# Kernel tuning notes

Measured on AMD Instinct MI355X. Metric: run time of the kernel, lower is better.

## Reference

```python
import jax, jax.numpy as jnp
import numpy as np

B, T, D, N = 16, 1024, 1024, 64
H = D // N          # 16 heads
DW, DA, DG = 64, 64, 160   # fla RWKV7 LoRA dims for D=1024
EPS = 64e-5         # GroupNorm eps = head_dim * 1e-5


def setup_inputs() -> dict:
    key = jax.random.key(0)
    ks = iter(jax.random.split(key, 40))
    def nrm(shape, s=0.02):
        return jax.random.normal(next(ks), shape, dtype=jnp.float32) * s
    inp = {
        "x": jax.random.normal(next(ks), (B, T, D), dtype=jnp.float32),
        # token-shift mixing coefficients
        "x_r": nrm((D,)), "x_w": nrm((D,)), "x_k": nrm((D,)),
        "x_v": nrm((D,)), "x_a": nrm((D,)), "x_g": nrm((D,)),
        # projections (no bias)
        "W_r": nrm((D, D)), "W_k": nrm((D, D)), "W_v": nrm((D, D)), "W_o": nrm((D, D)),
        # decay LoRA
        "w0": nrm((D,)), "w1": nrm((D, DW)), "w2": nrm((DW, D)),
        # in-context-lr LoRA
        "a0": nrm((D,)), "a1": nrm((D, DA)), "a2": nrm((DA, D)),
        # gate LoRA
        "g1": nrm((D, DG)), "g2": nrm((DG, D)),
        # per-channel key modifiers and per-head bonus
        "k_k": jnp.ones((D,), jnp.float32) * 0.85,
        "k_a": jnp.ones((D,), jnp.float32),
        "r_k": nrm((H, N)),
        # per-head GroupNorm affine
        "gn_w": jnp.ones((D,), jnp.float32), "gn_b": jnp.zeros((D,), jnp.float32),
        # classifier head
        "W_cls": nrm((D, 2)), "b_cls": jnp.zeros((2,), jnp.float32),
    }
    return inp


def rwkv7_scan(r, w, k, v, a, b):
    """RWKV7 delta-rule recurrence. All inputs [B,T,H,N]. Returns [B,T,H,N].
    S_t = S_{t-1} * diag(exp(-exp(w_t))) + (S_{t-1} a_t) b_t^T + v_t k_t^T
    o_t = S_t r_t
    """
    decay = jnp.exp(-jnp.exp(w))
    def step(S, inp):
        r_t, d_t, k_t, v_t, a_t, b_t = inp  # each [B,H,N]
        sa = jnp.einsum('bhij,bhj->bhi', S, a_t)
        S = (S * d_t[:, :, None, :]
             + sa[..., None] * b_t[:, :, None, :]
             + v_t[..., None] * k_t[:, :, None, :])
        o_t = jnp.einsum('bhij,bhj->bhi', S, r_t)
        return S, o_t
    xs = tuple(jnp.moveaxis(u, 1, 0) for u in (r, decay, k, v, a, b))
    S0 = jnp.zeros((r.shape[0], H, N, N), jnp.float32)
    _, o = jax.lax.scan(step, S0, xs)
    return jnp.moveaxis(o, 0, 1)


def reference(x, x_r, x_w, x_k, x_v, x_a, x_g,
              W_r, W_k, W_v, W_o,
              w0, w1, w2, a0, a1, a2, g1, g2,
              k_k, k_a, r_k, gn_w, gn_b, W_cls, b_cls):
    Bx, Tx, Dx = x.shape
    # token shift: delta = x_{t-1} - x_t (x_{-1} = 0)
    xprev = jnp.pad(x, ((0, 0), (1, 0), (0, 0)))[:, :-1]
    delta = xprev - x
    xr = x + delta * x_r
    xw = x + delta * x_w
    xk = x + delta * x_k
    xv = x + delta * x_v
    xa = x + delta * x_a
    xg = x + delta * x_g

    r = xr @ W_r
    k = xk @ W_k
    v = xv @ W_v   # layer 0: v_first = v, no value-residual mixing
    w = -jax.nn.softplus(-(w0 + jnp.tanh(xw @ w1) @ w2)) - 0.5
    a = jax.nn.sigmoid(a0 + (xa @ a1) @ a2)
    g = jax.nn.sigmoid(xg @ g1) @ g2

    kk = (k * k_k).reshape(Bx, Tx, H, N)
    kk = kk / jnp.maximum(jnp.linalg.norm(kk, axis=-1, keepdims=True), 1e-12)
    k = k * (1.0 + (a - 1.0) * k_a)

    rh = r.reshape(Bx, Tx, H, N)
    kh = k.reshape(Bx, Tx, H, N)
    vh = v.reshape(Bx, Tx, H, N)
    ah = a.reshape(Bx, Tx, H, N)
    wh = w.reshape(Bx, Tx, H, N)

    o = rwkv7_scan(rh, wh, kh, vh, -kk, kk * ah)

    # per-head GroupNorm (num_groups = H over channels D)
    mu = o.mean(-1, keepdims=True)
    var = o.var(-1, keepdims=True)
    o = (o - mu) / jnp.sqrt(var + EPS)
    o = o * gn_w.reshape(H, N) + gn_b.reshape(H, N)

    # per-head bonus term
    o = o + (rh * kh * r_k).sum(-1, keepdims=True) * vh
    o = (o.reshape(Bx, Tx, Dx) * g) @ W_o

    # TextRWKV head: max-pool over time, relu, (dropout=eval noop), linear
    h = jax.nn.relu(jnp.max(o, axis=1))
    return h @ W_cls + b_cls
```

## Files before the change

kernel.cpp:

```cpp
#include <hip/hip_runtime.h>
#include <hip/hip_bf16.h>

typedef unsigned short u16;
typedef unsigned int u32;

#define Bb 16
#define Tt 1024
#define Dd 1024
#define Nn 64
#define Hh 16
#define Mm (Bb*Tt)

#define TILE_M 64
#define TILE_N 64
#define TILE_K 16

typedef float f32x4 __attribute__((ext_vector_type(4)));
typedef short s16x8 __attribute__((ext_vector_type(8)));

struct __align__(8) u16x4s { u16 x, y, z, w; };

__device__ __forceinline__ float bf2f(u16 u) { return __uint_as_float(((u32)u) << 16); }
__device__ __forceinline__ u16 f2bf(float f) {
    __hip_bfloat16 h = __float2bfloat16(f);
    return *reinterpret_cast<u16*>(&h);
}
__device__ __forceinline__ float sigf(float x) { return 1.0f / (1.0f + expf(-x)); }

__global__ __launch_bounds__(256)
void mix6_kernel(const float* __restrict__ x,
                 const float* __restrict__ cr, const float* __restrict__ ck,
                 const float* __restrict__ cv, const float* __restrict__ cw,
                 const float* __restrict__ ca, const float* __restrict__ cg,
                 u16* __restrict__ o0, u16* __restrict__ o1, u16* __restrict__ o2,
                 u16* __restrict__ o3, u16* __restrict__ o4, u16* __restrict__ o5)
{
    const int m = blockIdx.x;
    const int c0 = threadIdx.x * 4;
    const size_t base = (size_t)m * Dd + c0;
    float4 xc = *(const float4*)(x + base);
    float4 xp = make_float4(0.f, 0.f, 0.f, 0.f);
    if (m & (Tt - 1)) xp = *(const float4*)(x + base - Dd);
    float dx[4] = {xp.x - xc.x, xp.y - xc.y, xp.z - xc.z, xp.w - xc.w};
    float xv[4] = {xc.x, xc.y, xc.z, xc.w};
    const float* cfs[6] = {cr, ck, cv, cw, ca, cg};
    u16* outs[6] = {o0, o1, o2, o3, o4, o5};
#pragma unroll
    for (int s = 0; s < 6; ++s) {
        float4 cf = *(const float4*)(cfs[s] + c0);
        float c4[4] = {cf.x, cf.y, cf.z, cf.w};
        u16x4s ov;
        u16* op = &ov.x;
#pragma unroll
        for (int l = 0; l < 4; ++l) op[l] = f2bf(fmaf(dx[l], c4[l], xv[l]));
        *(u16x4s*)(outs[s] + base) = ov;
    }
}

__global__ __launch_bounds__(256)
void sgemm_small(const u16* __restrict__ A, int lda,
                 const float* __restrict__ Bw, int ldb,
                 u16* __restrict__ C, int ldc,
                 int N, int K, int act)
{
    __shared__ float As[TILE_K][TILE_M + 1];
    __shared__ float Bs[TILE_K][TILE_N + 1];
    const int tid = threadIdx.x;
    const int tx = tid & 15, ty = tid >> 4;
    const int bm = blockIdx.x * TILE_M;
    const int bn = blockIdx.y * TILE_N;

    float acc[4][4] = {};

    for (int k0 = 0; k0 < K; k0 += TILE_K) {
#pragma unroll
        for (int l = 0; l < 4; ++l) {
            int idx = l * 256 + tid;
            int kk = idx & 15, mm = idx >> 4;
            As[kk][mm] = bf2f(A[(size_t)(bm + mm) * lda + k0 + kk]);
        }
#pragma unroll
        for (int l = 0; l < 4; ++l) {
            int idx = l * 256 + tid;
            int nn = idx & 63, kk = idx >> 6;
            int gn = bn + nn;
            Bs[kk][nn] = (gn < N) ? Bw[(size_t)(k0 + kk) * ldb + gn] : 0.0f;
        }
        __syncthreads();
#pragma unroll
        for (int kk = 0; kk < TILE_K; ++kk) {
            float af[4], bf[4];
#pragma unroll
            for (int i = 0; i < 4; ++i) af[i] = As[kk][ty * 4 + i];
#pragma unroll
            for (int j = 0; j < 4; ++j) bf[j] = Bs[kk][tx * 4 + j];
#pragma unroll
            for (int i = 0; i < 4; ++i)
#pragma unroll
                for (int j = 0; j < 4; ++j)
                    acc[i][j] = fmaf(af[i], bf[j], acc[i][j]);
        }
        __syncthreads();
    }

#pragma unroll
    for (int i = 0; i < 4; ++i) {
        int gm = bm + ty * 4 + i;
#pragma unroll
        for (int j = 0; j < 4; ++j) {
            int gn = bn + tx * 4 + j;
            if (gn >= N) continue;
            float v = acc[i][j];
            if (act == 1) v = tanhf(v);
            else if (act == 2) v = sigf(v);
            C[(size_t)gm * ldc + gn] = f2bf(v);
        }
    }
}

template<int ACT, bool HAS_BIAS>
__global__ __launch_bounds__(256)
void gemm_mfma(const u16* __restrict__ A, int lda,
               const float* __restrict__ W,
               const float* __restrict__ bias,
               u16* __restrict__ C, int K)
{
    __shared__ u16 As[128][40];
    __shared__ u16 Bs[128][40];
    const int tid = threadIdx.x;
    const int bm = blockIdx.x * 128, bn = blockIdx.y * 128;
    const int lane = tid & 63, w = tid >> 6;
    const int wr = w >> 1, wc = w & 1;
    const int lr = lane & 15, kg = lane >> 4;

    f32x4 acc[4][4];
#pragma unroll
    for (int m = 0; m < 4; ++m)
#pragma unroll
        for (int n = 0; n < 4; ++n) acc[m][n] = (f32x4){0.f, 0.f, 0.f, 0.f};

    for (int k0 = 0; k0 < K; k0 += 32) {
        {
            int row = tid >> 2, part = tid & 3;
            *(s16x8*)&As[row][part * 8] =
                *(const s16x8*)(A + (size_t)(bm + row) * lda + k0 + part * 8);
            row += 64;
            *(s16x8*)&As[row][part * 8] =
                *(const s16x8*)(A + (size_t)(bm + row) * lda + k0 + part * 8);
        }
        {
            int n4 = (tid & 31) * 4;
            int kp = tid >> 5;
#pragma unroll
            for (int it = 0; it < 2; ++it) {
                int k = 2 * (kp + it * 8);
                const float* wp = W + (size_t)(k0 + k) * 1024 + bn + n4;
                float4 wa = *(const float4*)wp;
                float4 wb = *(const float4*)(wp + 1024);
                *(u32*)&Bs[n4 + 0][k] = (u32)f2bf(wa.x) | ((u32)f2bf(wb.x) << 16);
                *(u32*)&Bs[n4 + 1][k] = (u32)f2bf(wa.y) | ((u32)f2bf(wb.y) << 16);
                *(u32*)&Bs[n4 + 2][k] = (u32)f2bf(wa.z) | ((u32)f2bf(wb.z) << 16);
                *(u32*)&Bs[n4 + 3][k] = (u32)f2bf(wa.w) | ((u32)f2bf(wb.w) << 16);
            }
        }
        __syncthreads();
        s16x8 af[4], bfr[4];
#pragma unroll
        for (int m = 0; m < 4; ++m)
            af[m] = *(const s16x8*)&As[wr * 64 + m * 16 + lr][kg * 8];
#pragma unroll
        for (int n = 0; n < 4; ++n)
            bfr[n] = *(const s16x8*)&Bs[wc * 64 + n * 16 + lr][kg * 8];
#pragma unroll
        for (int m = 0; m < 4; ++m)
#pragma unroll
            for (int n = 0; n < 4; ++n)
                acc[m][n] = __builtin_amdgcn_mfma_f32_16x16x32_bf16(af[m], bfr[n], acc[m][n], 0, 0, 0);
        __syncthreads();
    }

#pragma unroll
    for (int n = 0; n < 4; ++n) {
        int col = bn + wc * 64 + n * 16 + lr;
        float bv = HAS_BIAS ? bias[col] : 0.0f;
#pragma unroll
        for (int m = 0; m < 4; ++m) {
            int row0 = bm + wr * 64 + m * 16 + kg * 4;
#pragma unroll
            for (int r = 0; r < 4; ++r) {
                float v = acc[m][n][r] + bv;
                if (ACT == 2) v = sigf(v);
                else if (ACT == 3) {
                    float ww = -log1pf(expf(-v)) - 0.5f;
                    v = expf(-expf(ww));
                }
                C[(size_t)(row0 + r) * 1024 + col] = f2bf(v);
            }
        }
    }
}

__global__ __launch_bounds__(256)
void gemm_wo_mfma(const u16* __restrict__ A,
                  const float* __restrict__ W,
                  float* __restrict__ Hbuf)
{
    __shared__ u16 As[128][40];
    __shared__ u16 Bs[128][40];
    const int tid = threadIdx.x;
    const int bm = blockIdx.x * 128, bn = blockIdx.y * 128;
    const int lane = tid & 63, w = tid >> 6;
    const int wr = w >> 1, wc = w & 1;
    const int lr = lane & 15, kg = lane >> 4;

    f32x4 acc[4][4];
#pragma unroll
    for (int m = 0; m < 4; ++m)
#pragma unroll
        for (int n = 0; n < 4; ++n) acc[m][n] = (f32x4){0.f, 0.f, 0.f, 0.f};

    for (int k0 = 0; k0 < 1024; k0 += 32) {
        {
            int row = tid >> 2, part = tid & 3;
            *(s16x8*)&As[row][part * 8] =
                *(const s16x8*)(A + (size_t)(bm + row) * 1024 + k0 + part * 8);
            row += 64;
            *(s16x8*)&As[row][part * 8] =
                *(const s16x8*)(A + (size_t)(bm + row) * 1024 + k0 + part * 8);
        }
        {
            int n4 = (tid & 31) * 4;
            int kp = tid >> 5;
#pragma unroll
            for (int it = 0; it < 2; ++it) {
                int k = 2 * (kp + it * 8);
                const float* wp = W + (size_t)(k0 + k) * 1024 + bn + n4;
                float4 wa = *(const float4*)wp;
                float4 wb = *(const float4*)(wp + 1024);
                *(u32*)&Bs[n4 + 0][k] = (u32)f2bf(wa.x) | ((u32)f2bf(wb.x) << 16);
                *(u32*)&Bs[n4 + 1][k] = (u32)f2bf(wa.y) | ((u32)f2bf(wb.y) << 16);
                *(u32*)&Bs[n4 + 2][k] = (u32)f2bf(wa.z) | ((u32)f2bf(wb.z) << 16);
                *(u32*)&Bs[n4 + 3][k] = (u32)f2bf(wa.w) | ((u32)f2bf(wb.w) << 16);
            }
        }
        __syncthreads();
        s16x8 af[4], bfr[4];
#pragma unroll
        for (int m = 0; m < 4; ++m)
            af[m] = *(const s16x8*)&As[wr * 64 + m * 16 + lr][kg * 8];
#pragma unroll
        for (int n = 0; n < 4; ++n)
            bfr[n] = *(const s16x8*)&Bs[wc * 64 + n * 16 + lr][kg * 8];
#pragma unroll
        for (int m = 0; m < 4; ++m)
#pragma unroll
            for (int n = 0; n < 4; ++n)
                acc[m][n] = __builtin_amdgcn_mfma_f32_16x16x32_bf16(af[m], bfr[n], acc[m][n], 0, 0, 0);
        __syncthreads();
    }

    const int b = bm >> 10;
#pragma unroll
    for (int n = 0; n < 4; ++n) {
        float mv = -1e30f;
#pragma unroll
        for (int m = 0; m < 4; ++m)
#pragma unroll
            for (int r = 0; r < 4; ++r) mv = fmaxf(mv, acc[m][n][r]);
        mv = fmaxf(mv, __shfl_xor(mv, 16));
        mv = fmaxf(mv, __shfl_xor(mv, 32));
        mv = fmaxf(mv, 0.0f);
        if (lane < 16) {
            int col = bn + wc * 64 + n * 16 + lr;
            atomicMax((u32*)&Hbuf[b * Dd + col], __float_as_uint(mv));
        }
    }
}

__global__ __launch_bounds__(256)
void ew_kv_kernel(u16* __restrict__ kbuf, u16* __restrict__ abuf,
                  u16* __restrict__ kkbuf,
                  const float* __restrict__ k_k, const float* __restrict__ k_a)
{
    const int m = blockIdx.x;
    const int tid = threadIdx.x;
    const int c0 = tid * 4;
    const size_t base = (size_t)m * Dd + c0;
    u16x4s kv4 = *(const u16x4s*)(kbuf + base);
    u16x4s av4 = *(const u16x4s*)(abuf + base);
    float4 kkc = *(const float4*)(k_k + c0);
    float4 kac = *(const float4*)(k_a + c0);

    float kin[4] = {bf2f(kv4.x), bf2f(kv4.y), bf2f(kv4.z), bf2f(kv4.w)};
    float ain[4] = {bf2f(av4.x), bf2f(av4.y), bf2f(av4.z), bf2f(av4.w)};
    float kkc4[4] = {kkc.x, kkc.y, kkc.z, kkc.w};
    float kac4[4] = {kac.x, kac.y, kac.z, kac.w};

    float kr[4];
#pragma unroll
    for (int l = 0; l < 4; ++l) kr[l] = kin[l] * kkc4[l];
    float ss = kr[0]*kr[0] + kr[1]*kr[1] + kr[2]*kr[2] + kr[3]*kr[3];
#pragma unroll
    for (int mask = 1; mask < 16; mask <<= 1) ss += __shfl_xor(ss, mask);
    float inv = 1.0f / fmaxf(sqrtf(ss), 1e-12f);

    u16x4s kkv, kmv, bvv;
    u16* kkp = &kkv.x; u16* kmp = &kmv.x; u16* bvp = &bvv.x;
#pragma unroll
    for (int l = 0; l < 4; ++l) {
        float kkf = kr[l] * inv;
        kkp[l] = f2bf(kkf);
        kmp[l] = f2bf(kin[l] * (1.0f + (ain[l] - 1.0f) * kac4[l]));
        bvp[l] = f2bf(kkf * ain[l]);
    }
    *(u16x4s*)(kkbuf + base) = kkv;
    *(u16x4s*)(kbuf  + base) = kmv;
    *(u16x4s*)(abuf  + base) = bvv;
}

__global__ __launch_bounds__(256)
void scan_kernel(const u16* __restrict__ rb, const u16* __restrict__ db,
                 const u16* __restrict__ kb, const u16* __restrict__ vb,
                 const u16* __restrict__ kkb, const u16* __restrict__ bvb,
                 u16* __restrict__ ob)
{
    const int blk = blockIdx.x;
    const int batch = blk >> 4, head = blk & 15;
    const int tid = threadIdx.x;
    const int w = tid >> 6;
    const int lane = tid & 63;
    const int q = lane & 3, il = lane >> 2;
    const int i = w * 16 + il;
    const int j0 = q * 16;

    __shared__ float ws[4][2][6][64];

    const size_t rowbase = (size_t)batch * Tt * Dd + head * Nn;

    float S[16];
#pragma unroll
    for (int jj = 0; jj < 16; ++jj) S[jj] = 0.0f;

    {
        size_t off = rowbase + lane;
        ws[w][0][0][lane] = bf2f(rb[off]);
        ws[w][0][1][lane] = bf2f(db[off]);
        ws[w][0][2][lane] = bf2f(kb[off]);
        ws[w][0][3][lane] = bf2f(vb[off]);
        ws[w][0][4][lane] = bf2f(kkb[off]);
        ws[w][0][5][lane] = bf2f(bvb[off]);
    }
    u16 p0 = 0, p1 = 0, p2 = 0, p3 = 0, p4 = 0, p5 = 0;
    {
        size_t off = rowbase + Dd + lane;
        p0 = rb[off]; p1 = db[off]; p2 = kb[off];
        p3 = vb[off]; p4 = kkb[off]; p5 = bvb[off];
    }

    int c = 0;
    for (int t = 0; t < Tt; ++t) {
        if (t + 1 < Tt) {
            ws[w][c ^ 1][0][lane] = bf2f(p0);
            ws[w][c ^ 1][1][lane] = bf2f(p1);
            ws[w][c ^ 1][2][lane] = bf2f(p2);
            ws[w][c ^ 1][3][lane] = bf2f(p3);
            ws[w][c ^ 1][4][lane] = bf2f(p4);
            ws[w][c ^ 1][5][lane] = bf2f(p5);
        }
        if (t + 2 < Tt) {
            size_t off = rowbase + (size_t)(t + 2) * Dd + lane;
            p0 = rb[off]; p1 = db[off]; p2 = kb[off];
            p3 = vb[off]; p4 = kkb[off]; p5 = bvb[off];
        }

        float rv[16], dec[16], kv[16], kkv[16], bv[16];
#pragma unroll
        for (int u = 0; u < 4; ++u) {
            *(float4*)&rv[u*4]  = *(const float4*)&ws[w][c][0][j0 + u*4];
            *(float4*)&dec[u*4] = *(const float4*)&ws[w][c][1][j0 + u*4];
            *(float4*)&kv[u*4]  = *(const float4*)&ws[w][c][2][j0 + u*4];
            *(float4*)&kkv[u*4] = *(const float4*)&ws[w][c][4][j0 + u*4];
            *(float4*)&bv[u*4]  = *(const float4*)&ws[w][c][5][j0 + u*4];
        }
        float vi = ws[w][c][3][i];

        float sa = 0.0f;
#pragma unroll
        for (int jj = 0; jj < 16; ++jj) sa = fmaf(S[jj], kkv[jj], sa);
        sa = -sa;
        sa += __shfl_xor(sa, 1);
        sa += __shfl_xor(sa, 2);

        float op = 0.0f;
#pragma unroll
        for (int jj = 0; jj < 16; ++jj) {
            float Sv = S[jj] * dec[jj];
            Sv = fmaf(sa, bv[jj], Sv);
            Sv = fmaf(vi, kv[jj], Sv);
            S[jj] = Sv;
            op = fmaf(Sv, rv[jj], op);
        }
        op += __shfl_xor(op, 1);
        op += __shfl_xor(op, 2);
        if (q == 0) ob[rowbase + (size_t)t * Dd + i] = f2bf(op);

        c ^= 1;
    }
}

__global__ __launch_bounds__(256)
void gn_kernel(const u16* __restrict__ ob, const u16* __restrict__ rb,
               const u16* __restrict__ kb, const u16* __restrict__ vb,
               const u16* __restrict__ gb,
               const float* __restrict__ gn_w, const float* __restrict__ gn_b,
               const float* __restrict__ r_k, u16* __restrict__ o2)
{
    const int m = blockIdx.x;
    const int tid = threadIdx.x;
    const int c0 = tid * 4;
    const int h = tid >> 4;
    const int jh = c0 & 63;
    const size_t base = (size_t)m * Dd + c0;

    u16x4s ov4 = *(const u16x4s*)(ob + base);
    u16x4s rv4 = *(const u16x4s*)(rb + base);
    u16x4s kv4 = *(const u16x4s*)(kb + base);
    u16x4s vv4 = *(const u16x4s*)(vb + base);
    u16x4s gv4 = *(const u16x4s*)(gb + base);
    float4 rkc = *(const float4*)(r_k + h * 64 + jh);

    float ovv[4] = {bf2f(ov4.x), bf2f(ov4.y), bf2f(ov4.z), bf2f(ov4.w)};
    float rv[4] = {bf2f(rv4.x), bf2f(rv4.y), bf2f(rv4.z), bf2f(rv4.w)};
    float kv[4] = {bf2f(kv4.x), bf2f(kv4.y), bf2f(kv4.z), bf2f(kv4.w)};
    float vv[4] = {bf2f(vv4.x), bf2f(vv4.y), bf2f(vv4.z), bf2f(vv4.w)};
    float gv[4] = {bf2f(gv4.x), bf2f(gv4.y), bf2f(gv4.z), bf2f(gv4.w)};
    float rk4[4] = {rkc.x, rkc.y, rkc.z, rkc.w};

    float s1 = ovv[0] + ovv[1] + ovv[2] + ovv[3];
    float s2 = ovv[0]*ovv[0] + ovv[1]*ovv[1] + ovv[2]*ovv[2] + ovv[3]*ovv[3];
    float sb = rv[0]*kv[0]*rk4[0] + rv[1]*kv[1]*rk4[1] + rv[2]*kv[2]*rk4[2] + rv[3]*kv[3]*rk4[3];
#pragma unroll
    for (int mask = 1; mask < 16; mask <<= 1) {
        s1 += __shfl_xor(s1, mask);
        s2 += __shfl_xor(s2, mask);
        sb += __shfl_xor(sb, mask);
    }
    float mu = s1 * (1.0f / 64.0f);
    float var = s2 * (1.0f / 64.0f) - mu * mu;
    float rstd = rsqrtf(var + 6.4e-4f);

    float4 gwv = *(const float4*)(gn_w + c0);
    float4 gbv = *(const float4*)(gn_b + c0);
    float gw4[4] = {gwv.x, gwv.y, gwv.z, gwv.w};
    float gb4[4] = {gbv.x, gbv.y, gbv.z, gbv.w};

    u16x4s outv; u16* op = &outv.x;
#pragma unroll
    for (int l = 0; l < 4; ++l) {
        float v = (((ovv[l] - mu) * rstd) * gw4[l] + gb4[l] + sb * vv[l]) * gv[l];
        op[l] = f2bf(v);
    }
    *(u16x4s*)(o2 + base) = outv;
}

__global__ __launch_bounds__(256)
void zero_kernel(float* __restrict__ p, int n)
{
    int i = blockIdx.x * 256 + threadIdx.x;
    if (i < n) p[i] = 0.0f;
}

__global__ __launch_bounds__(256)
void cls_kernel(const float* __restrict__ hp, const float* __restrict__ Wc,
                const float* __restrict__ bc, float* __restrict__ out)
{
    const int p = blockIdx.x;
    const int b = p >> 1, c = p & 1;
    const int tid = threadIdx.x;
    float partial = 0.0f;
    for (int d = tid; d < Dd; d += 256)
        partial = fmaf(hp[b * Dd + d], Wc[d * 2 + c], partial);
    __shared__ float red[256];
    red[tid] = partial;
    __syncthreads();
    for (int s = 128; s > 0; s >>= 1) {
        if (tid < s) red[tid] += red[tid + s];
        __syncthreads();
    }
    if (tid == 0) out[b * 2 + c] = red[0] + bc[c];
}

extern "C" void kernel_launch(void* const* d_in, const int* in_sizes, int n_in,
                              void* d_out, int out_size, void* d_ws, size_t ws_size,
                              hipStream_t stream)
{
    const float* x    = (const float*)d_in[0];
    const float* x_r  = (const float*)d_in[1];
    const float* x_w  = (const float*)d_in[2];
    const float* x_k  = (const float*)d_in[3];
    const float* x_v  = (const float*)d_in[4];
    const float* x_a  = (const float*)d_in[5];
    const float* x_g  = (const float*)d_in[6];
    const float* W_r  = (const float*)d_in[7];
    const float* W_k  = (const float*)d_in[8];
    const float* W_v  = (const float*)d_in[9];
    const float* W_o  = (const float*)d_in[10];
    const float* w0   = (const float*)d_in[11];
    const float* w1   = (const float*)d_in[12];
    const float* w2   = (const float*)d_in[13];
    const float* a0   = (const float*)d_in[14];
    const float* a1   = (const float*)d_in[15];
    const float* a2   = (const float*)d_in[16];
    const float* g1   = (const float*)d_in[17];
    const float* g2   = (const float*)d_in[18];
    const float* k_k  = (const float*)d_in[19];
    const float* k_a  = (const float*)d_in[20];
    const float* r_k  = (const float*)d_in[21];
    const float* gn_w = (const float*)d_in[22];
    const float* gn_b = (const float*)d_in[23];
    const float* Wcls = (const float*)d_in[24];
    const float* bcls = (const float*)d_in[25];
    float* out = (float*)d_out;

    const size_t MD = (size_t)Mm * Dd;
    char* w = (char*)d_ws;
    u16* S0 = (u16*)w; w += MD * 2;
    u16* S1 = (u16*)w; w += MD * 2;
    u16* S2 = (u16*)w; w += MD * 2;
    u16* S3 = (u16*)w; w += MD * 2;
    u16* S4 = (u16*)w; w += MD * 2;
    u16* S5 = (u16*)w; w += MD * 2;
    u16* S6 = (u16*)w; w += MD * 2;
    u16* TW = (u16*)w; w += (size_t)Mm * 64 * 2;
    u16* TA = (u16*)w; w += (size_t)Mm * 64 * 2;
    u16* TG = (u16*)w; w += (size_t)Mm * 160 * 2;
    float* bufH = (float*)w; w += (size_t)Bb * Dd * 4;

    dim3 blk(256);
    dim3 gMix(Mm);
    dim3 gMf(Mm / 128, 1024 / 128);
    dim3 g64(Mm / TILE_M, 1);
    dim3 g160(Mm / TILE_M, 3);

    mix6_kernel<<<gMix, blk, 0, stream>>>(x, x_r, x_k, x_v, x_w, x_a, x_g,
                                          S0, S1, S2, S3, S4, S5);
    sgemm_small<<<g64,  blk, 0, stream>>>(S3, Dd, w1, 64,  TW, 64,  64,  Dd, 1);
    sgemm_small<<<g64,  blk, 0, stream>>>(S4, Dd, a1, 64,  TA, 64,  64,  Dd, 0);
    sgemm_small<<<g160, blk, 0, stream>>>(S5, Dd, g1, 160, TG, 160, 160, Dd, 2);
    gemm_mfma<0, false><<<gMf, blk, 0, stream>>>(S0, Dd, W_r, nullptr, S3, Dd);
    gemm_mfma<0, false><<<gMf, blk, 0, stream>>>(S1, Dd, W_k, nullptr, S4, Dd);
    gemm_mfma<0, false><<<gMf, blk, 0, stream>>>(S2, Dd, W_v, nullptr, S5, Dd);
    gemm_mfma<3, true><<<gMf, blk, 0, stream>>>(TW, 64, w2, w0, S0, 64);
    gemm_mfma<2, true><<<gMf, blk, 0, stream>>>(TA, 64, a2, a0, S1, 64);
    ew_kv_kernel<<<Mm, blk, 0, stream>>>(S4, S1, S2, k_k, k_a);
    scan_kernel<<<Bb * Hh, blk, 0, stream>>>(S3, S0, S4, S5, S2, S1, S6);
    gemm_mfma<0, false><<<gMf, blk, 0, stream>>>(TG, 160, g2, nullptr, S0, 160);
    gn_kernel<<<Mm, blk, 0, stream>>>(S6, S3, S4, S5, S0, gn_w, gn_b, r_k, S2);
    zero_kernel<<<(Bb * Dd + 255) / 256, blk, 0, stream>>>(bufH, Bb * Dd);
    gemm_wo_mfma<<<gMf, blk, 0, stream>>>(S2, W_o, bufH);
    cls_kernel<<<32, blk, 0, stream>>>(bufH, Wcls, bcls, out);
}
```

Before: 1.941 ms.

## Load scan inputs directly into registers, dropping LDS staging

The RWKV7 scan kernel no longer stages each timestep's r/decay/k/v/kk/b vectors through shared memory. Each lane now loads its 16-element bf16 slices straight from global memory as 16-byte vector loads, prefetched two steps ahead in registers, and converts them inline. This removes the LDS write/read traffic and the per-step staging work from the serial recurrence loop. In exchange, each lane issues redundant global loads of the same data and needs more registers for the two-deep prefetch buffers.

```diff
diff --git a/kernel.cpp b/kernel.cpp
--- a/kernel.cpp
+++ b/kernel.cpp
@@ -19,6 +19,7 @@
 typedef short s16x8 __attribute__((ext_vector_type(8)));
 
 struct __align__(8) u16x4s { u16 x, y, z, w; };
+struct slice16 { s16x8 lo, hi; };
 
 __device__ __forceinline__ float bf2f(u16 u) { return __uint_as_float(((u32)u) << 16); }
 __device__ __forceinline__ u16 f2bf(float f) {
@@ -26,6 +27,13 @@
     return *reinterpret_cast<u16*>(&h);
 }
 __device__ __forceinline__ float sigf(float x) { return 1.0f / (1.0f + expf(-x)); }
+
+__device__ __forceinline__ slice16 ldslice(const u16* p) {
+    slice16 s;
+    s.lo = *(const s16x8*)p;
+    s.hi = *(const s16x8*)(p + 8);
+    return s;
+}
 
 __global__ __launch_bounds__(256)
 void mix6_kernel(const float* __restrict__ x,
@@ -333,78 +341,74 @@
     const int i = w * 16 + il;
     const int j0 = q * 16;
 
-    __shared__ float ws[4][2][6][64];
-
     const size_t rowbase = (size_t)batch * Tt * Dd + head * Nn;
 
     float S[16];
 #pragma unroll
     for (int jj = 0; jj < 16; ++jj) S[jj] = 0.0f;
 
+    slice16 cr, cd, ck_, cc, cb;
+    u16 cv;
     {
-        size_t off = rowbase + lane;
-        ws[w][0][0][lane] = bf2f(rb[off]);
-        ws[w][0][1][lane] = bf2f(db[off]);
-        ws[w][0][2][lane] = bf2f(kb[off]);
-        ws[w][0][3][lane] = bf2f(vb[off]);
-        ws[w][0][4][lane] = bf2f(kkb[off]);
-        ws[w][0][5][lane] = bf2f(bvb[off]);
-    }
-    u16 p0 = 0, p1 = 0, p2 = 0, p3 = 0, p4 = 0, p5 = 0;
-    {
-        size_t off = rowbase + Dd + lane;
-        p0 = rb[off]; p1 = db[off]; p2 = kb[off];
-        p3 = vb[off]; p4 = kkb[off]; p5 = bvb[off];
-    }
-
-    int c = 0;
+        size_t o = rowbase + j0;
+        cr = ldslice(rb + o); cd = ldslice(db + o); ck_ = ldslice(kb + o);
+        cc = ldslice(kkb + o); cb = ldslice(bvb + o);
+        cv = vb[rowbase + i];
+    }
+    slice16 nr = cr, nd = cd, nk = ck_, nc = cc, nb = cb;
+    u16 nv = cv;
+    if (Tt > 1) {
+        size_t o = rowbase + Dd + j0;
+        nr = ldslice(rb + o); nd = ldslice(db + o); nk = ldslice(kb + o);
+        nc = ldslice(kkb + o); nb = ldslice(bvb + o);
+        nv = vb[rowbase + Dd + i];
+    }
+
     for (int t = 0; t < Tt; ++t) {
-        if (t + 1 < Tt) {
-            ws[w][c ^ 1][0][lane] = bf2f(p0);
-            ws[w][c ^ 1][1][lane] = bf2f(p1);
-            ws[w][c ^ 1][2][lane] = bf2f(p2);
-            ws[w][c ^ 1][3][lane] = bf2f(p3);
-            ws[w][c ^ 1][4][lane] = bf2f(p4);
-            ws[w][c ^ 1][5][lane] = bf2f(p5);
-        }
+        slice16 mr = nr, md = nd, mk = nk, mc = nc, mb = nb;
+        u16 mv = nv;
         if (t + 2 < Tt) {
-            size_t off = rowbase + (size_t)(t + 2) * Dd + lane;
-            p0 = rb[off]; p1 = db[off]; p2 = kb[off];
-            p3 = vb[off]; p4 = kkb[off]; p5 = bvb[off];
-        }
-
-        float rv[16], dec[16], kv[16], kkv[16], bv[16];
-#pragma unroll
-        for (int u = 0; u < 4; ++u) {
-            *(float4*)&rv[u*4]  = *(const float4*)&ws[w][c][0][j0 + u*4];
-            *(float4*)&dec[u*4] = *(const float4*)&ws[w][c][1][j0 + u*4];
-            *(float4*)&kv[u*4]  = *(const float4*)&ws[w][c][2][j0 + u*4];
-            *(float4*)&kkv[u*4] = *(const float4*)&ws[w][c][4][j0 + u*4];
-            *(float4*)&bv[u*4]  = *(const float4*)&ws[w][c][5][j0 + u*4];
-        }
-        float vi = ws[w][c][3][i];
+            size_t o = rowbase + (size_t)(t + 2) * Dd;
+            mr = ldslice(rb + o + j0); md = ldslice(db + o + j0);
+            mk = ldslice(kb + o + j0); mc = ldslice(kkb + o + j0);
+            mb = ldslice(bvb + o + j0);
+            mv = vb[o + i];
+        }
+
+        float vi = bf2f(cv);
 
         float sa = 0.0f;
 #pragma unroll
-        for (int jj = 0; jj < 16; ++jj) sa = fmaf(S[jj], kkv[jj], sa);
+        for (int jj = 0; jj < 8; ++jj) sa = fmaf(S[jj], bf2f((u16)cc.lo[jj]), sa);
+#pragma unroll
+        for (int jj = 0; jj < 8; ++jj) sa = fmaf(S[8 + jj], bf2f((u16)cc.hi[jj]), sa);
         sa = -sa;
         sa += __shfl_xor(sa, 1);
         sa += __shfl_xor(sa, 2);
 
         float op = 0.0f;
 #pragma unroll
-        for (int jj = 0; jj < 16; ++jj) {
-            float Sv = S[jj] * dec[jj];
-            Sv = fmaf(sa, bv[jj], Sv);
-            Sv = fmaf(vi, kv[jj], Sv);
+        for (int jj = 0; jj < 8; ++jj) {
+            float Sv = S[jj] * bf2f((u16)cd.lo[jj]);
+            Sv = fmaf(sa, bf2f((u16)cb.lo[jj]), Sv);
+            Sv = fmaf(vi, bf2f((u16)ck_.lo[jj]), Sv);
             S[jj] = Sv;
-            op = fmaf(Sv, rv[jj], op);
+            op = fmaf(Sv, bf2f((u16)cr.lo[jj]), op);
+        }
+#pragma unroll
+        for (int jj = 0; jj < 8; ++jj) {
+            float Sv = S[8 + jj] * bf2f((u16)cd.hi[jj]);
+            Sv = fmaf(sa, bf2f((u16)cb.hi[jj]), Sv);
+            Sv = fmaf(vi, bf2f((u16)ck_.hi[jj]), Sv);
+            S[8 + jj] = Sv;
+            op = fmaf(Sv, bf2f((u16)cr.hi[jj]), op);
         }
         op += __shfl_xor(op, 1);
         op += __shfl_xor(op, 2);
         if (q == 0) ob[rowbase + (size_t)t * Dd + i] = f2bf(op);
 
-        c ^= 1;
+        cr = nr; cd = nd; ck_ = nk; cc = nc; cb = nb; cv = nv;
+        nr = mr; nd = md; nk = mk; nc = mc; nb = mb; nv = mv;
     }
 }
 
```

Result: slower. 2.060 ms (+6.1%).
